# Kernel tuning notes

Hardware: AMD Instinct MI355X
Metric: run time of the kernel (lower is better)

## Reference

```python
import jax, jax.numpy as jnp
import numpy as np

# 8-bit signed symmetric quantization grid (bit buffer in the module is set to 8 at runtime)
SAT_MAX = 127.0
SAT_MIN = -127.0


def _squant_stage(rn, re, un, ue, up_p, dn, de, dn_p):
    """One SQuant flip stage over the last axis (vectorized SQuant_func).

    For each row: e = sum(rounding_error); flip round(|e|) elements.
    If e < 0 (under-rounded overall) flip the highest-up-priority elements up,
    else flip the highest-down-priority elements down. The boundary (last,
    lowest-priority flipped) element gets a nonzero priority in the opposite
    direction so the next (coarser) stage can revert it — this reproduces the
    in-place priority update SQuant_func performs after zeroing priorities.
    All tensors have shape [..., K].
    """
    e_sum = jnp.sum(re, axis=-1)                                   # [...]
    n_flip = jnp.round(jnp.abs(e_sum)).astype(jnp.int32)[..., None]  # [...,1]
    flip_up = (e_sum < 0)[..., None]                               # [...,1]
    prio = jnp.where(flip_up, up_p, dn_p)
    order = jnp.argsort(-prio, axis=-1)        # descending priority
    rank = jnp.argsort(order, axis=-1)         # rank[i] = position of i in order
    mask = rank < n_flip                       # elements to flip
    rn2 = jnp.where(mask, jnp.where(flip_up, un, dn), rn)
    re2 = jnp.where(mask, jnp.where(flip_up, ue, de), re)
    # boundary element (rank == n_flip-1) gets opposite-direction priority
    boundary = mask & (rank == (n_flip - 1))
    b_prio = jnp.where(boundary, jnp.abs(re2), 0.0)
    up_p2 = jnp.where(flip_up, jnp.zeros_like(b_prio), b_prio)
    dn_p2 = jnp.where(flip_up, b_prio, jnp.zeros_like(b_prio))
    return rn2, re2, up_p2, dn_p2


def adaptive_round(x, t_min, t_max):
    rn = jnp.round(x)
    re = rn - x
    # up candidates: elements rounded down (re < 0) and not saturated high
    ue = jnp.where((x >= t_max) | (re > 0), 0.0, re)
    up_p = jnp.abs(ue)
    nz_u = ue != 0
    ue = jnp.where(nz_u, ue + 1.0, ue)
    un = jnp.where(nz_u, rn + 1.0, rn)
    # down candidates: elements rounded up (re > 0) and not saturated low
    de = jnp.where((x <= t_min) | (re < 0), 0.0, re)
    dn_p = jnp.abs(de)
    nz_d = de != 0
    de = jnp.where(nz_d, de - 1.0, de)
    dn = jnp.where(nz_d, rn - 1.0, rn)

    OC, IC = x.shape[0], x.shape[1]
    K = x.size // (OC * IC)
    shp_k = (OC, IC, K)         # squant-k: per (oc, ic) kernel row
    rn_k, re_k, up_p_k, dn_p_k = _squant_stage(
        rn.reshape(shp_k), re.reshape(shp_k),
        un.reshape(shp_k), ue.reshape(shp_k), up_p.reshape(shp_k),
        dn.reshape(shp_k), de.reshape(shp_k), dn_p.reshape(shp_k))
    shp_c = (1, OC, IC * K)     # squant-c: per oc channel row
    rn_c, _, _, _ = _squant_stage(
        rn_k.reshape(shp_c), re_k.reshape(shp_c),
        un.reshape(shp_c), ue.reshape(shp_c), up_p_k.reshape(shp_c),
        dn.reshape(shp_c), de.reshape(shp_c), dn_p_k.reshape(shp_c))
    return rn_c.reshape(x.shape)


def setup_inputs() -> dict:
    key = jax.random.key(0)
    tensor = jax.random.normal(key, (1024, 1024, 3, 3), dtype=jnp.float32)
    return {"tensor": tensor}


def reference(tensor) -> jnp.ndarray:
    # symmetric linear quantization params from tensor min/max (weight path)
    max_abs = jnp.maximum(jnp.abs(jnp.max(tensor)), jnp.abs(jnp.min(tensor)))
    scale = max_abs / SAT_MAX                       # element scale
    q = jnp.clip(tensor / scale, SAT_MIN, SAT_MAX)  # linear_quantize
    q = adaptive_round(q, SAT_MIN, SAT_MAX)         # SQuant adaptive rounding
    return q * scale                                # linear_dequantize
```

## Files before the change

kernel.cpp:

```cpp
#include <hip/hip_runtime.h>

#define OC 1024
#define ICN 1024
#define KK 9
#define NELEM (OC * ICN * KK)
#define CH (ICN * KK)
#define CH4 (CH / 4)
#define BT 512
#define KMB 1024

__global__ void __launch_bounds__(256) kmax_part(const float* __restrict__ x,
                                                 float* __restrict__ part) {
    __shared__ float s_m[4];
    const int tid = blockIdx.x * 256 + threadIdx.x;
    const int stride = KMB * 256;
    const float4* x4 = (const float4*)x;
    float m = 0.f;
    #pragma unroll
    for (int k = 0; k < 9; ++k) {
        float4 v = x4[tid + k * stride];
        m = fmaxf(m, fmaxf(fmaxf(fabsf(v.x), fabsf(v.y)), fmaxf(fabsf(v.z), fabsf(v.w))));
    }
    #pragma unroll
    for (int off = 32; off > 0; off >>= 1)
        m = fmaxf(m, __shfl_xor(m, off, 64));
    if ((threadIdx.x & 63) == 0) s_m[threadIdx.x >> 6] = m;
    __syncthreads();
    if (threadIdx.x == 0)
        part[blockIdx.x] = fmaxf(fmaxf(s_m[0], s_m[1]), fmaxf(s_m[2], s_m[3]));
}

__global__ void __launch_bounds__(256) kmax_atomic(const float* __restrict__ x,
                                                   unsigned* __restrict__ ws) {
    __shared__ float s_m[4];
    const int tid = blockIdx.x * 256 + threadIdx.x;
    const int stride = KMB * 256;
    const float4* x4 = (const float4*)x;
    float m = 0.f;
    #pragma unroll
    for (int k = 0; k < 9; ++k) {
        float4 v = x4[tid + k * stride];
        m = fmaxf(m, fmaxf(fmaxf(fabsf(v.x), fabsf(v.y)), fmaxf(fabsf(v.z), fabsf(v.w))));
    }
    #pragma unroll
    for (int off = 32; off > 0; off >>= 1)
        m = fmaxf(m, __shfl_xor(m, off, 64));
    if ((threadIdx.x & 63) == 0) s_m[threadIdx.x >> 6] = m;
    __syncthreads();
    if (threadIdx.x == 0) {
        m = fmaxf(fmaxf(s_m[0], s_m[1]), fmaxf(s_m[2], s_m[3]));
        atomicMax(ws, __float_as_uint(m));
    }
}

template <int C>
__device__ __forceinline__ void red_step(unsigned& key, unsigned& row) {
    unsigned k2 = (unsigned)__builtin_amdgcn_update_dpp(0, (int)key, C, 0xF, 0xF, false);
    unsigned r2 = (unsigned)__builtin_amdgcn_update_dpp(0, (int)row, C, 0xF, 0xF, false);
    if (k2 >= key) { key = k2; row = r2; }
}

__device__ __forceinline__ void wave_argmax(unsigned& key, unsigned& row) {
    red_step<0x111>(key, row);
    red_step<0x112>(key, row);
    red_step<0x114>(key, row);
    red_step<0x118>(key, row);
    red_step<0x142>(key, row);
    red_step<0x143>(key, row);
}

__global__ void __launch_bounds__(BT, 8) squant_kernel(const float* __restrict__ x,
                                                       float* __restrict__ out,
                                                       const float* __restrict__ part,
                                                       int nparts) {
    __shared__ __align__(16) short s_q[CH];
    __shared__ float s_res[ICN];
    __shared__ float s_prio[ICN];
    __shared__ int   s_meta[ICN];
    __shared__ float s_mx[8];

    const int oc = blockIdx.x;
    const int t  = threadIdx.x;
    const long long ocbase = (long long)oc * CH;

    float m;
    if (nparts > 0) {
        m = fmaxf(part[t], part[t + BT]);
        #pragma unroll
        for (int off = 32; off > 0; off >>= 1)
            m = fmaxf(m, __shfl_xor(m, off, 64));
        if ((t & 63) == 0) s_mx[t >> 6] = m;
    } else if (t == 0) {
        s_mx[0] = __uint_as_float(((const unsigned*)part)[0]);
    }
    __syncthreads();
    if (nparts > 0) {
        m = s_mx[0];
        #pragma unroll
        for (int w = 1; w < 8; ++w) m = fmaxf(m, s_mx[w]);
    } else {
        m = s_mx[0];
    }
    const float scale = m / 127.0f;
    const float iscale = 1.0f / scale;

    #pragma unroll
    for (int half = 0; half < 2; ++half) {
        const int row = t + half * BT;
        const float* px = x + ocbase + row * KK;
        float rn[KK], re[KK];
        float e = 0.f;
        #pragma unroll
        for (int k = 0; k < KK; ++k) {
            float q = px[k] * iscale;
            q = fminf(fmaxf(q, -127.f), 127.f);
            float r = rintf(q);
            rn[k] = r;
            re[k] = r - q;
            e += re[k];
        }
        int nf = (int)rintf(fabsf(e));
        bool up = e < 0.f;
        unsigned flipped = 0u;
        int bidx = -1;
        float b_re = 0.f;
        for (int f = 0; f < nf; ++f) {
            float bp = 0.f; int bk = -1; float cre = 0.f;
            #pragma unroll
            for (int k = 0; k < KK; ++k) {
                bool cand = up ? (re[k] < 0.f) : (re[k] > 0.f);
                float p = (cand && !((flipped >> k) & 1u)) ? fabsf(re[k]) : 0.f;
                if (p > bp) { bp = p; bk = k; cre = re[k]; }
            }
            if (bk < 0) break;
            flipped |= (1u << bk);
            bidx = bk; b_re = cre;
        }
        int cnt = __popc(flipped);
        float sgn = up ? 1.f : -1.f;

        #pragma unroll
        for (int k = 0; k < KK; ++k) {
            float v = rn[k] + (((flipped >> k) & 1u) ? sgn : 0.f);
            s_q[row * KK + k] = (short)(int)v;
        }
        s_res[row] = e + sgn * (float)cnt;
        if (bidx >= 0) {
            s_prio[row] = fabsf(b_re + sgn);
            s_meta[row] = (row * KK + bidx) | ((up ? 1 : 0) << 16);
        } else {
            s_prio[row] = 0.f;
            s_meta[row] = 0;
        }
    }
    __syncthreads();

    if (t < 64) {
        float s = 0.f;
        #pragma unroll
        for (int i = 0; i < ICN / 64; ++i) s += s_res[t + i * 64];
        #pragma unroll
        for (int off = 32; off > 0; off >>= 1) s += __shfl_xor(s, off, 64);

        int n2 = (int)rintf(fabsf(s));
        bool up2 = s < 0.f;
        if (n2 > 0) {
            unsigned k[ICN / 64];
            #pragma unroll
            for (int i = 0; i < ICN / 64; ++i) {
                int r = t + i * 64;
                float pr = s_prio[r];
                int dir = s_meta[r] >> 16;
                bool match = ((dir != 0) != up2);
                unsigned bits = __float_as_uint(pr);
                k[i] = (pr > 0.f && match)
                         ? (((bits - 0x3F000000u + 1u) << 4) | (15u - (unsigned)i))
                         : 0u;
            }
            unsigned bk = 0u;
            #pragma unroll
            for (int i = 0; i < ICN / 64; ++i) bk = (k[i] > bk) ? k[i] : bk;
            unsigned brow = (unsigned)(t + (15 - (int)(bk & 15u)) * 64);

            unsigned fmask = 0u;
            int f = 0;
            for (; f < n2; ++f) {
                unsigned key = bk, row = brow;
                wave_argmax(key, row);
                unsigned kw = (unsigned)__builtin_amdgcn_readlane((int)key, 63);
                unsigned rw = (unsigned)__builtin_amdgcn_readlane((int)row, 63);
                if (kw == 0u) break;
                int iw = 15 - (int)(kw & 15u);
                bool owner = (t == (int)(rw & 63u));
                if (owner) fmask |= (1u << iw);
                unsigned zm = owner ? (1u << iw) : 0u;
                unsigned nb = 0u;
                #pragma unroll
                for (int i = 0; i < ICN / 64; ++i) {
                    unsigned ki = ((zm >> i) & 1u) ? 0u : k[i];
                    k[i] = ki;
                    nb = (ki > nb) ? ki : nb;
                }
                bk = nb;
                brow = (unsigned)(t + (15 - (int)(bk & 15u)) * 64);
            }

            #pragma unroll
            for (int i = 0; i < ICN / 64; ++i) {
                if ((fmask >> i) & 1u) {
                    int meta = s_meta[t + i * 64];
                    int gid = meta & 0xFFFF;
                    s_q[gid] = (short)(s_q[gid] + ((meta >> 16) ? -1 : 1));
                }
            }

            if (f < n2) {
                int remaining = n2 - f;
                if (remaining > CH) remaining = CH;
                for (int j = t; j < remaining; j += 64) {
                    float q = x[ocbase + j] * iscale;
                    q = fminf(fmaxf(q, -127.f), 127.f);
                    float r = rintf(q);
                    float rr = r - q;
                    float v = up2 ? ((rr < 0.f) ? r + 1.f : r)
                                  : ((rr > 0.f) ? r - 1.f : r);
                    s_q[j] = (short)(int)v;
                }
            }
        }
    }
    __syncthreads();

    const short4* q4 = (const short4*)s_q;
    float4* o4 = (float4*)(out + ocbase);
    for (int i = t; i < CH4; i += BT) {
        short4 v = q4[i];
        float4 o;
        o.x = (float)v.x * scale;
        o.y = (float)v.y * scale;
        o.z = (float)v.z * scale;
        o.w = (float)v.w * scale;
        o4[i] = o;
    }
}

extern "C" void kernel_launch(void* const* d_in, const int* in_sizes, int n_in,
                              void* d_out, int out_size, void* d_ws, size_t ws_size,
                              hipStream_t stream) {
    const float* x = (const float*)d_in[0];
    float* out = (float*)d_out;
    if (ws_size >= KMB * sizeof(float)) {
        float* part = (float*)d_ws;
        kmax_part<<<KMB, 256, 0, stream>>>(x, part);
        squant_kernel<<<OC, BT, 0, stream>>>(x, out, part, KMB);
    } else {
        unsigned* wsmax = (unsigned*)d_ws;
        hipMemsetAsync(d_ws, 0, 4, stream);
        kmax_atomic<<<KMB, 256, 0, stream>>>(x, wsmax);
        squant_kernel<<<OC, BT, 0, stream>>>(x, out, (const float*)d_ws, 0);
    }
}
```

Before: 102.6 us.

## Fuse global max reduction into squant kernel via cooperative grid sync

Replaces the separate max-partial kernel plus squant kernel with one cooperative kernel. Each block computes the abs-max of its own output channel, writes it to the workspace, does a grid-wide sync, reduces all partials, then runs the shared squant core. This removes a kernel launch and a full extra read pass over the input, since each block's channel rows are likely still in cache when it rounds them. In exchange it needs all 1024 blocks co-resident and pays for a grid barrier, and it falls back to the two-kernel path if occupancy or cooperative launch is unavailable.

Result: no change. 103.6 us (+1.0%).

```diff
diff --git a/kernel.cpp b/kernel.cpp
--- a/kernel.cpp
+++ b/kernel.cpp
@@ -1,4 +1,7 @@
 #include <hip/hip_runtime.h>
+#include <hip/hip_cooperative_groups.h>
+
+namespace cg = cooperative_groups;
 
 #define OC 1024
 #define ICN 1024
@@ -69,40 +72,16 @@
     red_step<0x143>(key, row);
 }
 
-__global__ void __launch_bounds__(BT, 8) squant_kernel(const float* __restrict__ x,
-                                                       float* __restrict__ out,
-                                                       const float* __restrict__ part,
-                                                       int nparts) {
+__device__ __forceinline__ void squant_core(const float* __restrict__ x,
+                                            float* __restrict__ out,
+                                            int oc, float scale, float iscale) {
     __shared__ __align__(16) short s_q[CH];
     __shared__ float s_res[ICN];
     __shared__ float s_prio[ICN];
     __shared__ int   s_meta[ICN];
-    __shared__ float s_mx[8];
-
-    const int oc = blockIdx.x;
-    const int t  = threadIdx.x;
+
+    const int t = threadIdx.x;
     const long long ocbase = (long long)oc * CH;
-
-    float m;
-    if (nparts > 0) {
-        m = fmaxf(part[t], part[t + BT]);
-        #pragma unroll
-        for (int off = 32; off > 0; off >>= 1)
-            m = fmaxf(m, __shfl_xor(m, off, 64));
-        if ((t & 63) == 0) s_mx[t >> 6] = m;
-    } else if (t == 0) {
-        s_mx[0] = __uint_as_float(((const unsigned*)part)[0]);
-    }
-    __syncthreads();
-    if (nparts > 0) {
-        m = s_mx[0];
-        #pragma unroll
-        for (int w = 1; w < 8; ++w) m = fmaxf(m, s_mx[w]);
-    } else {
-        m = s_mx[0];
-    }
-    const float scale = m / 127.0f;
-    const float iscale = 1.0f / scale;
 
     #pragma unroll
     for (int half = 0; half < 2; ++half) {
@@ -244,6 +223,83 @@
     }
 }
 
+__global__ void __launch_bounds__(BT, 8) squant_coop(const float* __restrict__ x,
+                                                     float* __restrict__ out,
+                                                     float* __restrict__ part) {
+    __shared__ float s_mx[8];
+    const int oc = blockIdx.x;
+    const int t  = threadIdx.x;
+    const long long ocbase = (long long)oc * CH;
+
+    const float4* x4 = (const float4*)(x + ocbase);
+    float m = 0.f;
+    #pragma unroll
+    for (int i = 0; i < 5; ++i) {
+        int idx = t + i * BT;
+        if (idx < CH4) {
+            float4 v = x4[idx];
+            m = fmaxf(m, fmaxf(fmaxf(fabsf(v.x), fabsf(v.y)), fmaxf(fabsf(v.z), fabsf(v.w))));
+        }
+    }
+    #pragma unroll
+    for (int off = 32; off > 0; off >>= 1)
+        m = fmaxf(m, __shfl_xor(m, off, 64));
+    if ((t & 63) == 0) s_mx[t >> 6] = m;
+    __syncthreads();
+    if (t == 0) {
+        float bm = s_mx[0];
+        #pragma unroll
+        for (int w = 1; w < 8; ++w) bm = fmaxf(bm, s_mx[w]);
+        part[oc] = bm;
+        __threadfence();
+    }
+    cg::this_grid().sync();
+    __threadfence();
+
+    float pm = fmaxf(part[t], part[t + BT]);
+    #pragma unroll
+    for (int off = 32; off > 0; off >>= 1)
+        pm = fmaxf(pm, __shfl_xor(pm, off, 64));
+    if ((t & 63) == 0) s_mx[t >> 6] = pm;
+    __syncthreads();
+    pm = s_mx[0];
+    #pragma unroll
+    for (int w = 1; w < 8; ++w) pm = fmaxf(pm, s_mx[w]);
+
+    const float scale = pm / 127.0f;
+    const float iscale = 1.0f / scale;
+    squant_core(x, out, oc, scale, iscale);
+}
+
+__global__ void __launch_bounds__(BT, 8) squant_kernel(const float* __restrict__ x,
+                                                       float* __restrict__ out,
+                                                       const float* __restrict__ part,
+                                                       int nparts) {
+    __shared__ float s_mx[8];
+    const int t = threadIdx.x;
+    float m;
+    if (nparts > 0) {
+        m = fmaxf(part[t], part[t + BT]);
+        #pragma unroll
+        for (int off = 32; off > 0; off >>= 1)
+            m = fmaxf(m, __shfl_xor(m, off, 64));
+        if ((t & 63) == 0) s_mx[t >> 6] = m;
+    } else if (t == 0) {
+        s_mx[0] = __uint_as_float(((const unsigned*)part)[0]);
+    }
+    __syncthreads();
+    if (nparts > 0) {
+        m = s_mx[0];
+        #pragma unroll
+        for (int w = 1; w < 8; ++w) m = fmaxf(m, s_mx[w]);
+    } else {
+        m = s_mx[0];
+    }
+    const float scale = m / 127.0f;
+    const float iscale = 1.0f / scale;
+    squant_core(x, out, blockIdx.x, scale, iscale);
+}
+
 extern "C" void kernel_launch(void* const* d_in, const int* in_sizes, int n_in,
                               void* d_out, int out_size, void* d_ws, size_t ws_size,
                               hipStream_t stream) {
@@ -251,6 +307,26 @@
     float* out = (float*)d_out;
     if (ws_size >= KMB * sizeof(float)) {
         float* part = (float*)d_ws;
+        static int coop = -1;
+        if (coop < 0) {
+            int dev = 0, attr = 0, nblk = 0, ncu = 0;
+            hipGetDevice(&dev);
+            hipDeviceGetAttribute(&attr, hipDeviceAttributeCooperativeLaunch, dev);
+            if (attr) {
+                hipOccupancyMaxActiveBlocksPerMultiprocessor(&nblk, squant_coop, BT, 0);
+                hipDeviceGetAttribute(&ncu, hipDeviceAttributeMultiprocessorCount, dev);
+                coop = (nblk * ncu >= OC) ? 1 : 0;
+            } else {
+                coop = 0;
+            }
+        }
+        if (coop == 1) {
+            void* args[] = {(void*)&x, (void*)&out, (void*)&part};
+            hipError_t e = hipLaunchCooperativeKernel(squant_coop, dim3(OC), dim3(BT),
+                                                      args, 0u, stream);
+            if (e == hipSuccess) return;
+            coop = 0;
+        }
         kmax_part<<<KMB, 256, 0, stream>>>(x, part);
         squant_kernel<<<OC, BT, 0, stream>>>(x, out, part, KMB);
     } else {
```
